# Kernel optimization log

Hardware: AMD Instinct MI355X
Metric: run time of the kernel (lower is better)

## Reference

```python
import jax, jax.numpy as jnp
import numpy as np

L = 128          # bandlimit (max_l)
NTHETA = 256     # Gauss-Legendre latitudes (>= L for exact quadrature)
NPHI = 512       # longitudes (>= 2L-1)
C_IN, C_OUT = 32, 32


def _normalized_assoc_legendre(Lmax, xg):
    """Pbar_lm(x) with Condon-Shortley phase, orthonormal on the sphere.
    Returns (Lmax, Lmax, T) for m>=0; zero for m>l."""
    T = xg.shape[0]
    P = np.zeros((Lmax, Lmax, T), dtype=np.float64)
    sx = np.sqrt(np.maximum(1.0 - xg * xg, 0.0))
    P[0, 0] = 1.0 / np.sqrt(4.0 * np.pi)
    for m in range(1, Lmax):
        P[m, m] = -np.sqrt((2 * m + 1) / (2.0 * m)) * sx * P[m - 1, m - 1]
    for m in range(0, Lmax - 1):
        P[m + 1, m] = np.sqrt(2 * m + 3.0) * xg * P[m, m]
    for m in range(Lmax):
        for l in range(m + 2, Lmax):
            a = np.sqrt((4.0 * l * l - 1.0) / (l * l - m * m))
            b = np.sqrt(((l - 1.0) ** 2 - m * m) / (4.0 * (l - 1.0) ** 2 - 1.0))
            P[l, m] = a * (xg * P[l - 1, m] - b * P[l - 2, m])
    return P


def _build_basis():
    # Gauss-Legendre quadrature in cos(theta): exact for degree <= 2*NTHETA-1
    xg, wg = np.polynomial.legendre.leggauss(NTHETA)
    P = _normalized_assoc_legendre(L, xg)  # (L, L, T), m>=0
    # Full basis B[l, m+L-1, t]; Pbar_{l,-m} = (-1)^m Pbar_{l,m}
    B = np.zeros((L, 2 * L - 1, NTHETA), dtype=np.float64)
    for m in range(-(L - 1), L):
        B[:, m + L - 1, :] = ((-1.0) ** abs(m) if m < 0 else 1.0) * P[:, abs(m), :]
    return B.astype(np.float32), wg.astype(np.float32)


def setup_inputs() -> dict:
    key = jax.random.key(0)
    k1, k2, k3 = jax.random.split(key, 3)
    x = jax.random.normal(k1, (NTHETA, NPHI, C_IN), dtype=jnp.float32)
    std = 1.0 / (C_IN + C_OUT)
    wr = std * jax.random.normal(k2, (L, 2 * L - 1, C_IN, C_OUT), dtype=jnp.float32)
    wi = std * jax.random.normal(k3, (L, 2 * L - 1, C_IN, C_OUT), dtype=jnp.float32)
    B, wg = _build_basis()
    return {"x": x, "weights_real": wr, "weights_imag": wi,
            "legendre": jnp.asarray(B), "quad_w": jnp.asarray(wg)}


def reference(x, weights_real, weights_imag, legendre, quad_w):
    ntheta, nphi, _ = x.shape
    Lb = legendre.shape[0]
    # --- forward SHT (per channel, vectorized) ---
    # longitude FFT: Fm[t,k,c] = sum_p x e^{-i 2pi k p / nphi}; dphi = 2pi/nphi
    Fm = jnp.fft.fft(x.astype(jnp.complex64), axis=1) * (2.0 * np.pi / nphi)
    midx = np.arange(-(Lb - 1), Lb) % nphi            # FFT bins for m=-(L-1)..L-1
    Fm_sel = Fm[:, midx, :]                           # (t, 2L-1, c)
    Bw = legendre * quad_w[None, None, :]             # quadrature-weighted basis
    # flm[l,m,c] = sum_t w_t Pbar_lm(theta_t) Fm[t,m,c]
    flm = jnp.einsum('lmt,tmc->lmc', Bw.astype(jnp.complex64), Fm_sel)
    # --- spectral conv: per-(l,m) channel mixing ---
    W = weights_real.astype(jnp.complex64) + 1j * weights_imag.astype(jnp.complex64)
    y = jnp.einsum('lmc,lmco->lmo', flm, W)           # (L, 2L-1, O)
    # --- inverse SHT ---
    G = jnp.einsum('lmt,lmo->tmo', legendre.astype(jnp.complex64), y)  # (t, 2L-1, O)
    spec = jnp.zeros((ntheta, nphi, G.shape[-1]), dtype=jnp.complex64)
    spec = spec.at[:, midx, :].set(G)
    out = jnp.fft.ifft(spec, axis=1) * nphi           # f = sum_m G e^{i m phi}
    return jnp.moveaxis(out.real, 2, 0)               # (O, ntheta, nphi)
```

## Files before the change

### kernel.cpp

```cpp
#include <hip/hip_runtime.h>
#include <math.h>

#define DEVFN __global__ __launch_bounds__(256)

namespace {
constexpr int LL  = 128;
constexpr int MM2 = 255;
constexpr int NT  = 256;
constexpr int NP  = 512;
constexpr int NC  = 32;
constexpr int NO  = 32;
constexpr float TWO_PI = 6.283185307179586476925286766559f;
}

typedef short v8s __attribute__((ext_vector_type(8)));
typedef float v4f __attribute__((ext_vector_type(4)));

__device__ inline unsigned short f2bf(float f) {
  unsigned int u = __float_as_uint(f);
  return (unsigned short)((u + 0x7FFFu + ((u >> 16) & 1u)) >> 16);
}

__device__ inline int m_of(int k, int mloc) {
  return (mloc < 8) ? (8 * k + mloc) : (120 - 8 * k + (mloc - 8));
}

DEVFN void kp_prep(const float* __restrict__ x, unsigned short* __restrict__ tw1t,
                   unsigned short* __restrict__ vt, unsigned short* __restrict__ xb) {
  __shared__ float sm[32][65];
  const int bid = blockIdx.x;
  const int tid = threadIdx.x;
  const float phi = TWO_PI / (float)NP;
  if (bid < 512) {
    const int idx = bid * 256 + tid;
    const float fs = TWO_PI / (float)NP;
    {
      const int n = idx >> 9, p = idx & 511;
      const int m = n >> 1;
      const int k = (m * p) & (NP - 1);
      float s, c;
      sincosf(phi * (float)k, &s, &c);
      tw1t[idx] = f2bf((n & 1) ? (-s * fs) : (c * fs));
    }
    {
      const int p = idx >> 8, k = idx & 255;
      const int m = k >> 1;
      const int kk = (m * p) & (NP - 1);
      float s, c;
      sincosf(phi * (float)kk, &s, &c);
      vt[idx] = f2bf((k & 1) ? s : c);
    }
  } else {
    const int q = bid - 512;
    const int t = q >> 3;
    const int p0 = (q & 7) * 64;
#pragma unroll
    for (int i = 0; i < 8; ++i) {
      const int idx = tid + i * 256;
      const int p = idx >> 5, c = idx & 31;
      sm[c][p] = x[((size_t)t * NP + p0 + p) * NC + c];
    }
    __syncthreads();
    const int c = tid >> 3, pg = tid & 7;
    unsigned short pk[8];
#pragma unroll
    for (int u = 0; u < 8; ++u) pk[u] = f2bf(sm[c][pg * 8 + u]);
    *(uint4*)(xb + ((size_t)(t * 32 + c)) * NP + p0 + pg * 8) = *(const uint4*)pk;
  }
}

DEVFN void k1_mfma(const unsigned short* __restrict__ xb,
                   const unsigned short* __restrict__ tw1t,
                   const float* __restrict__ wg,
                   float* __restrict__ fwr, float* __restrict__ fwi) {
  __shared__ unsigned short As[128 * 32];
  __shared__ unsigned short Bs[64 * 32];
  const int tid = threadIdx.x;
  const int r0 = blockIdx.x * 128;
  const int n0 = blockIdx.y * 64;
  const int wid = tid >> 6, lane = tid & 63;
  const int wm = wid & 1, wn = wid >> 1;
  v4f acc[4][2];
#pragma unroll
  for (int i = 0; i < 4; ++i)
#pragma unroll
    for (int j = 0; j < 2; ++j) {
      acc[i][j][0] = 0.f; acc[i][j][1] = 0.f; acc[i][j][2] = 0.f; acc[i][j][3] = 0.f;
    }
  const int lr = lane & 15, lk = (lane >> 4) * 8;
  for (int k0 = 0; k0 < 512; k0 += 32) {
#pragma unroll
    for (int s = 0; s < 3; ++s) {
      const int chunk = tid + s * 256;
      if (chunk < 512) {
        const int row = chunk >> 2, c16 = chunk & 3;
        *(uint4*)&As[row * 32 + c16 * 8] =
            *(const uint4*)&xb[(size_t)(r0 + row) * 512 + k0 + c16 * 8];
      } else {
        const int bc = chunk - 512;
        const int row = bc >> 2, c16 = bc & 3;
        *(uint4*)&Bs[row * 32 + c16 * 8] =
            *(const uint4*)&tw1t[(size_t)(n0 + row) * 512 + k0 + c16 * 8];
      }
    }
    __syncthreads();
    v8s af[4], bf[2];
#pragma unroll
    for (int i = 0; i < 4; ++i) af[i] = *(const v8s*)&As[(wm * 64 + i * 16 + lr) * 32 + lk];
#pragma unroll
    for (int j = 0; j < 2; ++j) bf[j] = *(const v8s*)&Bs[(wn * 32 + j * 16 + lr) * 32 + lk];
#pragma unroll
    for (int i = 0; i < 4; ++i)
#pragma unroll
      for (int j = 0; j < 2; ++j)
        acc[i][j] = __builtin_amdgcn_mfma_f32_16x16x32_bf16(af[i], bf[j], acc[i][j], 0, 0, 0);
    __syncthreads();
  }
  const int lrow = (lane >> 4) * 4;
#pragma unroll
  for (int i = 0; i < 4; ++i) {
    const int rbase = r0 + wm * 64 + i * 16 + lrow;
    const int t = rbase >> 5, c0 = rbase & 31;
    const float w = wg[t];
#pragma unroll
    for (int j = 0; j < 2; ++j) {
      const int n = n0 + wn * 32 + j * 16 + lr;
      const int mI = n >> 1;
      float* dst = (n & 1) ? fwi : fwr;
      float4 v = {acc[i][j][0] * w, acc[i][j][1] * w, acc[i][j][2] * w, acc[i][j][3] * w};
      *(float4*)&dst[((size_t)mI * NT + t) * NC + c0] = v;
    }
  }
}

DEVFN void k2_flm(const float* __restrict__ leg, const float* __restrict__ fwr,
                  const float* __restrict__ fwi, float* __restrict__ flr,
                  float* __restrict__ fli) {
  const int m  = blockIdx.x;
  const int l0 = m + blockIdx.y * 8 + (threadIdx.x >> 6) * 2;
  if (l0 >= LL) return;
  const int lane = threadIdx.x & 63;
  const int c = lane & 31;
  const int l1 = min(l0 + 1, LL - 1);
  const float* fp = ((lane >> 5) ? fwi : fwr) + (size_t)m * NT * NC + c;
  const float* lgA = leg + ((size_t)(l0 * MM2 + 127 + m)) * NT;
  const float* lgB = leg + ((size_t)(l1 * MM2 + 127 + m)) * NT;
  float a0 = 0.f, a1 = 0.f;
#pragma unroll 4
  for (int t = 0; t < NT; t += 4) {
    const float f0 = fp[(t + 0) * NC];
    const float f1 = fp[(t + 1) * NC];
    const float f2 = fp[(t + 2) * NC];
    const float f3 = fp[(t + 3) * NC];
    const float4 bA = *(const float4*)(lgA + t);
    const float4 bB = *(const float4*)(lgB + t);
    a0 = fmaf(bA.x, f0, a0); a0 = fmaf(bA.y, f1, a0);
    a0 = fmaf(bA.z, f2, a0); a0 = fmaf(bA.w, f3, a0);
    a1 = fmaf(bB.x, f0, a1); a1 = fmaf(bB.y, f1, a1);
    a1 = fmaf(bB.z, f2, a1); a1 = fmaf(bB.w, f3, a1);
  }
  float* outp = (lane >> 5) ? fli : flr;
  outp[(size_t)(m * LL + l0) * NC + c] = a0;
  if (l0 + 1 < LL) outp[(size_t)(m * LL + l0 + 1) * NC + c] = a1;
}

DEVFN void k3_mix(const float* __restrict__ flr, const float* __restrict__ fli,
                  const float* __restrict__ wr, const float* __restrict__ wi,
                  float* __restrict__ ya, float* __restrict__ yb) {
  const int m  = blockIdx.x;
  const int wid = threadIdx.x >> 6, lane = threadIdx.x & 63;
  const int l = m + blockIdx.y * 4 + wid;
  if (l >= LL) return;
  const int c8 = lane >> 3;
  const int o8 = lane & 7;
  const int c0 = c8 * 4, o0 = o8 * 4;
  const float s0 = (m > 0) ? 1.0f : 0.0f;
  const size_t rp = ((size_t)(l * MM2 + 127 + m) * NC) * NO;
  const size_t rn = ((size_t)(l * MM2 + 127 - m) * NC) * NO;
  const float4 fa4 = *(const float4*)&flr[(size_t)(m * LL + l) * NC + c0];
  const float4 fb4 = *(const float4*)&fli[(size_t)(m * LL + l) * NC + c0];
  float4 accA = {0.f, 0.f, 0.f, 0.f}, accB = {0.f, 0.f, 0.f, 0.f};
#pragma unroll
  for (int i = 0; i < 4; ++i) {
    const int c = c0 + i;
    const float4 wrp = *(const float4*)&wr[rp + (size_t)c * NO + o0];
    const float4 wrn = *(const float4*)&wr[rn + (size_t)c * NO + o0];
    const float4 wip = *(const float4*)&wi[rp + (size_t)c * NO + o0];
    const float4 win = *(const float4*)&wi[rn + (size_t)c * NO + o0];
    const float fa = (i == 0) ? fa4.x : (i == 1) ? fa4.y : (i == 2) ? fa4.z : fa4.w;
    const float fb = (i == 0) ? fb4.x : (i == 1) ? fb4.y : (i == 2) ? fb4.z : fb4.w;
    float4 wa, wb;
    wa.x = fmaf(s0, wrn.x, wrp.x); wa.y = fmaf(s0, wrn.y, wrp.y);
    wa.z = fmaf(s0, wrn.z, wrp.z); wa.w = fmaf(s0, wrn.w, wrp.w);
    wb.x = fmaf(s0, win.x, -wip.x); wb.y = fmaf(s0, win.y, -wip.y);
    wb.z = fmaf(s0, win.z, -wip.z); wb.w = fmaf(s0, win.w, -wip.w);
    accA.x = fmaf(fa, wa.x, fmaf(fb, wb.x, accA.x));
    accA.y = fmaf(fa, wa.y, fmaf(fb, wb.y, accA.y));
    accA.z = fmaf(fa, wa.z, fmaf(fb, wb.z, accA.z));
    accA.w = fmaf(fa, wa.w, fmaf(fb, wb.w, accA.w));
    accB.x = fmaf(fa, wb.x, fmaf(-fb, wa.x, accB.x));
    accB.y = fmaf(fa, wb.y, fmaf(-fb, wa.y, accB.y));
    accB.z = fmaf(fa, wb.z, fmaf(-fb, wa.z, accB.z));
    accB.w = fmaf(fa, wb.w, fmaf(-fb, wa.w, accB.w));
  }
#pragma unroll
  for (int mask = 8; mask <= 32; mask <<= 1) {
    accA.x += __shfl_xor(accA.x, mask); accA.y += __shfl_xor(accA.y, mask);
    accA.z += __shfl_xor(accA.z, mask); accA.w += __shfl_xor(accA.w, mask);
    accB.x += __shfl_xor(accB.x, mask); accB.y += __shfl_xor(accB.y, mask);
    accB.z += __shfl_xor(accB.z, mask); accB.w += __shfl_xor(accB.w, mask);
  }
  if (c8 == 0) {
    *(float4*)&ya[(size_t)(m * LL + l) * NO + o0] = accA;
    *(float4*)&yb[(size_t)(m * LL + l) * NO + o0] = accB;
  }
}

DEVFN void k4_G(const float* __restrict__ leg, const float* __restrict__ ya,
                const float* __restrict__ yb, unsigned short* __restrict__ ut) {
  const int fid = blockIdx.x + (int)blockIdx.y * 128;
  const int xk  = fid & 7;
  const int loc = fid >> 3;
  const int m   = m_of(xk, loc >> 3);
  const int tc  = loc & 7;
  const int o = threadIdx.x & 31;
  const int tq = threadIdx.x >> 5;
  const int t0 = tc * 32 + tq * 4;
  float aa[4] = {}, bb[4] = {};
#pragma unroll 4
  for (int l = m; l < LL; ++l) {
    const float4 g = *(const float4*)(leg + ((size_t)(l * MM2 + 127 + m)) * NT + t0);
    const float yav = ya[(m * LL + l) * NO + o];
    const float ybv = yb[(m * LL + l) * NO + o];
    aa[0] = fmaf(g.x, yav, aa[0]);  bb[0] = fmaf(g.x, ybv, bb[0]);
    aa[1] = fmaf(g.y, yav, aa[1]);  bb[1] = fmaf(g.y, ybv, bb[1]);
    aa[2] = fmaf(g.z, yav, aa[2]);  bb[2] = fmaf(g.z, ybv, bb[2]);
    aa[3] = fmaf(g.w, yav, aa[3]);  bb[3] = fmaf(g.w, ybv, bb[3]);
  }
#pragma unroll
  for (int i = 0; i < 4; ++i) {
    const unsigned int pk = (unsigned int)f2bf(aa[i]) | ((unsigned int)f2bf(bb[i]) << 16);
    *(unsigned int*)&ut[((size_t)((t0 + i) * 32 + o)) * 256 + 2 * m] = pk;
  }
}

DEVFN void k5_mfma(const unsigned short* __restrict__ ut,
                   const unsigned short* __restrict__ vt,
                   float* __restrict__ out) {
  __shared__ unsigned short As[128 * 32];
  __shared__ unsigned short Bs[128 * 32];
  const int tid = threadIdx.x;
  const int p0 = blockIdx.x * 128;
  const int r0 = blockIdx.y * 128;
  const int wid = tid >> 6, lane = tid & 63;
  const int wm = wid & 1, wn = wid >> 1;
  v4f acc[4][4];
#pragma unroll
  for (int i = 0; i < 4; ++i)
#pragma unroll
    for (int j = 0; j < 4; ++j) {
      acc[i][j][0] = 0.f; acc[i][j][1] = 0.f; acc[i][j][2] = 0.f; acc[i][j][3] = 0.f;
    }
  const int lr = lane & 15, lk = (lane >> 4) * 8;
  for (int k0 = 0; k0 < 256; k0 += 32) {
#pragma unroll
    for (int s = 0; s < 2; ++s) {
      const int chunk = tid + s * 256;
      const int row = chunk >> 2, c16 = chunk & 3;
      *(uint4*)&As[row * 32 + c16 * 8] =
          *(const uint4*)&vt[(size_t)(p0 + row) * 256 + k0 + c16 * 8];
      *(uint4*)&Bs[row * 32 + c16 * 8] =
          *(const uint4*)&ut[(size_t)(r0 + row) * 256 + k0 + c16 * 8];
    }
    __syncthreads();
    v8s af[4], bf[4];
#pragma unroll
    for (int i = 0; i < 4; ++i) af[i] = *(const v8s*)&As[(wm * 64 + i * 16 + lr) * 32 + lk];
#pragma unroll
    for (int j = 0; j < 4; ++j) bf[j] = *(const v8s*)&Bs[(wn * 64 + j * 16 + lr) * 32 + lk];
#pragma unroll
    for (int i = 0; i < 4; ++i)
#pragma unroll
      for (int j = 0; j < 4; ++j)
        acc[i][j] = __builtin_amdgcn_mfma_f32_16x16x32_bf16(af[i], bf[j], acc[i][j], 0, 0, 0);
    __syncthreads();
  }
  const int lrow = (lane >> 4) * 4;
#pragma unroll
  for (int i = 0; i < 4; ++i) {
    const int pbase = p0 + wm * 64 + i * 16 + lrow;
#pragma unroll
    for (int j = 0; j < 4; ++j) {
      const int r = r0 + wn * 64 + j * 16 + lr;
      const int t = r >> 5, o = r & 31;
      float4 v = {acc[i][j][0], acc[i][j][1], acc[i][j][2], acc[i][j][3]};
      *(float4*)&out[((size_t)o * NT + t) * NP + pbase] = v;
    }
  }
}

extern "C" void kernel_launch(void* const* d_in, const int* in_sizes, int n_in,
                              void* d_out, int out_size, void* d_ws, size_t ws_size,
                              hipStream_t stream) {
  const float* x   = (const float*)d_in[0];
  const float* wr  = (const float*)d_in[1];
  const float* wi  = (const float*)d_in[2];
  const float* leg = (const float*)d_in[3];
  const float* wg  = (const float*)d_in[4];
  float* out = (float*)d_out;

  unsigned short* tw1t = (unsigned short*)d_ws;
  unsigned short* vt   = tw1t + 131072;
  unsigned short* xb   = vt + 131072;
  unsigned short* ut   = xb + 4194304;
  float* fwr = (float*)(ut + 2097152);
  float* fwi = fwr + 1048576;
  float* flr = fwi + 1048576;
  float* fli = flr + 524288;
  float* ya  = fli + 524288;
  float* yb  = ya + 524288;

  hipLaunchKernelGGL(kp_prep, dim3(2560), dim3(256), 0, stream, x, tw1t, vt, xb);
  hipLaunchKernelGGL(k1_mfma, dim3(64, 4), dim3(256), 0, stream, xb, tw1t, wg, fwr, fwi);
  hipLaunchKernelGGL(k2_flm, dim3(128, 16), dim3(256), 0, stream, leg, fwr, fwi, flr, fli);
  hipLaunchKernelGGL(k3_mix, dim3(128, 32), dim3(256), 0, stream, flr, fli, wr, wi, ya, yb);
  hipLaunchKernelGGL(k4_G, dim3(128, 8), dim3(256), 0, stream, leg, ya, yb, ut);
  hipLaunchKernelGGL(k5_mfma, dim3(4, 64), dim3(256), 0, stream, ut, vt, out);
}
```

Baseline: 364.8 us.

## Fuse forward Legendre, channel mix and inverse Legendre into one kernel

Replaces the separate flm, mixing and G kernels with one kernel per (m, l-residue-mod-4) block that holds flm and y in shared memory. The inverse Legendre partial sums for the four l-residue groups go to four fp32 slabs. The final MFMA kernel reduces these slabs and converts them to bf16 while staging its B tile. That kernel also changes its tile shape to 256x64. This removes two launches and the global round-trips for flm and y, at the cost of 4x partial-sum traffic. Each block's inner loop also runs longer and more serially, and with one block per (m, residue) and no triangle reordering, work per block is uneven across m.

New measurement: 417.7 us. 1.15x slower.

```diff
diff --git a/kernel.cpp b/kernel.cpp
--- a/kernel.cpp
+++ b/kernel.cpp
@@ -19,10 +19,6 @@
 __device__ inline unsigned short f2bf(float f) {
   unsigned int u = __float_as_uint(f);
   return (unsigned short)((u + 0x7FFFu + ((u >> 16) & 1u)) >> 16);
-}
-
-__device__ inline int m_of(int k, int mloc) {
-  return (mloc < 8) ? (8 * k + mloc) : (120 - 8 * k + (mloc - 8));
 }
 
 DEVFN void kp_prep(const float* __restrict__ x, unsigned short* __restrict__ tw1t,
@@ -133,127 +129,131 @@
   }
 }
 
-DEVFN void k2_flm(const float* __restrict__ leg, const float* __restrict__ fwr,
-                  const float* __restrict__ fwi, float* __restrict__ flr,
-                  float* __restrict__ fli) {
-  const int m  = blockIdx.x;
-  const int l0 = m + blockIdx.y * 8 + (threadIdx.x >> 6) * 2;
-  if (l0 >= LL) return;
-  const int lane = threadIdx.x & 63;
-  const int c = lane & 31;
-  const int l1 = min(l0 + 1, LL - 1);
-  const float* fp = ((lane >> 5) ? fwi : fwr) + (size_t)m * NT * NC + c;
-  const float* lgA = leg + ((size_t)(l0 * MM2 + 127 + m)) * NT;
-  const float* lgB = leg + ((size_t)(l1 * MM2 + 127 + m)) * NT;
-  float a0 = 0.f, a1 = 0.f;
-#pragma unroll 4
-  for (int t = 0; t < NT; t += 4) {
-    const float f0 = fp[(t + 0) * NC];
-    const float f1 = fp[(t + 1) * NC];
-    const float f2 = fp[(t + 2) * NC];
-    const float f3 = fp[(t + 3) * NC];
-    const float4 bA = *(const float4*)(lgA + t);
-    const float4 bB = *(const float4*)(lgB + t);
-    a0 = fmaf(bA.x, f0, a0); a0 = fmaf(bA.y, f1, a0);
-    a0 = fmaf(bA.z, f2, a0); a0 = fmaf(bA.w, f3, a0);
-    a1 = fmaf(bB.x, f0, a1); a1 = fmaf(bB.y, f1, a1);
-    a1 = fmaf(bB.z, f2, a1); a1 = fmaf(bB.w, f3, a1);
-  }
-  float* outp = (lane >> 5) ? fli : flr;
-  outp[(size_t)(m * LL + l0) * NC + c] = a0;
-  if (l0 + 1 < LL) outp[(size_t)(m * LL + l0 + 1) * NC + c] = a1;
-}
-
-DEVFN void k3_mix(const float* __restrict__ flr, const float* __restrict__ fli,
-                  const float* __restrict__ wr, const float* __restrict__ wi,
-                  float* __restrict__ ya, float* __restrict__ yb) {
-  const int m  = blockIdx.x;
-  const int wid = threadIdx.x >> 6, lane = threadIdx.x & 63;
-  const int l = m + blockIdx.y * 4 + wid;
-  if (l >= LL) return;
-  const int c8 = lane >> 3;
-  const int o8 = lane & 7;
-  const int c0 = c8 * 4, o0 = o8 * 4;
-  const float s0 = (m > 0) ? 1.0f : 0.0f;
-  const size_t rp = ((size_t)(l * MM2 + 127 + m) * NC) * NO;
-  const size_t rn = ((size_t)(l * MM2 + 127 - m) * NC) * NO;
-  const float4 fa4 = *(const float4*)&flr[(size_t)(m * LL + l) * NC + c0];
-  const float4 fb4 = *(const float4*)&fli[(size_t)(m * LL + l) * NC + c0];
-  float4 accA = {0.f, 0.f, 0.f, 0.f}, accB = {0.f, 0.f, 0.f, 0.f};
-#pragma unroll
-  for (int i = 0; i < 4; ++i) {
-    const int c = c0 + i;
-    const float4 wrp = *(const float4*)&wr[rp + (size_t)c * NO + o0];
-    const float4 wrn = *(const float4*)&wr[rn + (size_t)c * NO + o0];
-    const float4 wip = *(const float4*)&wi[rp + (size_t)c * NO + o0];
-    const float4 win = *(const float4*)&wi[rn + (size_t)c * NO + o0];
-    const float fa = (i == 0) ? fa4.x : (i == 1) ? fa4.y : (i == 2) ? fa4.z : fa4.w;
-    const float fb = (i == 0) ? fb4.x : (i == 1) ? fb4.y : (i == 2) ? fb4.z : fb4.w;
-    float4 wa, wb;
-    wa.x = fmaf(s0, wrn.x, wrp.x); wa.y = fmaf(s0, wrn.y, wrp.y);
-    wa.z = fmaf(s0, wrn.z, wrp.z); wa.w = fmaf(s0, wrn.w, wrp.w);
-    wb.x = fmaf(s0, win.x, -wip.x); wb.y = fmaf(s0, win.y, -wip.y);
-    wb.z = fmaf(s0, win.z, -wip.z); wb.w = fmaf(s0, win.w, -wip.w);
-    accA.x = fmaf(fa, wa.x, fmaf(fb, wb.x, accA.x));
-    accA.y = fmaf(fa, wa.y, fmaf(fb, wb.y, accA.y));
-    accA.z = fmaf(fa, wa.z, fmaf(fb, wb.z, accA.z));
-    accA.w = fmaf(fa, wa.w, fmaf(fb, wb.w, accA.w));
-    accB.x = fmaf(fa, wb.x, fmaf(-fb, wa.x, accB.x));
-    accB.y = fmaf(fa, wb.y, fmaf(-fb, wa.y, accB.y));
-    accB.z = fmaf(fa, wb.z, fmaf(-fb, wa.z, accB.z));
-    accB.w = fmaf(fa, wb.w, fmaf(-fb, wa.w, accB.w));
-  }
-#pragma unroll
-  for (int mask = 8; mask <= 32; mask <<= 1) {
-    accA.x += __shfl_xor(accA.x, mask); accA.y += __shfl_xor(accA.y, mask);
-    accA.z += __shfl_xor(accA.z, mask); accA.w += __shfl_xor(accA.w, mask);
-    accB.x += __shfl_xor(accB.x, mask); accB.y += __shfl_xor(accB.y, mask);
-    accB.z += __shfl_xor(accB.z, mask); accB.w += __shfl_xor(accB.w, mask);
-  }
-  if (c8 == 0) {
-    *(float4*)&ya[(size_t)(m * LL + l) * NO + o0] = accA;
-    *(float4*)&yb[(size_t)(m * LL + l) * NO + o0] = accB;
-  }
-}
-
-DEVFN void k4_G(const float* __restrict__ leg, const float* __restrict__ ya,
-                const float* __restrict__ yb, unsigned short* __restrict__ ut) {
-  const int fid = blockIdx.x + (int)blockIdx.y * 128;
-  const int xk  = fid & 7;
-  const int loc = fid >> 3;
-  const int m   = m_of(xk, loc >> 3);
-  const int tc  = loc & 7;
-  const int o = threadIdx.x & 31;
-  const int tq = threadIdx.x >> 5;
-  const int t0 = tc * 32 + tq * 4;
-  float aa[4] = {}, bb[4] = {};
-#pragma unroll 4
-  for (int l = m; l < LL; ++l) {
-    const float4 g = *(const float4*)(leg + ((size_t)(l * MM2 + 127 + m)) * NT + t0);
-    const float yav = ya[(m * LL + l) * NO + o];
-    const float ybv = yb[(m * LL + l) * NO + o];
-    aa[0] = fmaf(g.x, yav, aa[0]);  bb[0] = fmaf(g.x, ybv, bb[0]);
-    aa[1] = fmaf(g.y, yav, aa[1]);  bb[1] = fmaf(g.y, ybv, bb[1]);
-    aa[2] = fmaf(g.z, yav, aa[2]);  bb[2] = fmaf(g.z, ybv, bb[2]);
-    aa[3] = fmaf(g.w, yav, aa[3]);  bb[3] = fmaf(g.w, ybv, bb[3]);
-  }
-#pragma unroll
-  for (int i = 0; i < 4; ++i) {
-    const unsigned int pk = (unsigned int)f2bf(aa[i]) | ((unsigned int)f2bf(bb[i]) << 16);
-    *(unsigned int*)&ut[((size_t)((t0 + i) * 32 + o)) * 256 + 2 * m] = pk;
-  }
-}
-
-DEVFN void k5_mfma(const unsigned short* __restrict__ ut,
+__global__ __launch_bounds__(256, 2) void k23B(
+    const float* __restrict__ leg, const float* __restrict__ fwr,
+    const float* __restrict__ fwi, const float* __restrict__ wr,
+    const float* __restrict__ wi, float* __restrict__ gp) {
+  __shared__ float sflm[32][64];
+  __shared__ float sy[32][64];
+  const int bid = blockIdx.x;
+  const int m = bid >> 2, q = bid & 3;
+  const int tid = threadIdx.x;
+  const int wid = tid >> 6, lane = tid & 63;
+  const int jmin = (m > q) ? ((m - q + 3) >> 2) : 0;
+
+  {
+    const int c = lane & 31;
+    const float* fp = ((lane >> 5) ? fwi : fwr) + (size_t)m * NT * NC + c;
+    const float* lg[8];
+#pragma unroll
+    for (int k = 0; k < 8; ++k) {
+      const int l = q + 4 * (wid + 4 * k);
+      lg[k] = leg + ((size_t)(l * MM2 + 127 + m)) * NT;
+    }
+    float acc[8] = {};
+    for (int t = 0; t < NT; t += 4) {
+      const float f0 = fp[(t + 0) * NC];
+      const float f1 = fp[(t + 1) * NC];
+      const float f2 = fp[(t + 2) * NC];
+      const float f3 = fp[(t + 3) * NC];
+#pragma unroll
+      for (int k = 0; k < 8; ++k) {
+        const float4 b = *(const float4*)(lg[k] + t);
+        acc[k] = fmaf(b.x, f0, acc[k]);
+        acc[k] = fmaf(b.y, f1, acc[k]);
+        acc[k] = fmaf(b.z, f2, acc[k]);
+        acc[k] = fmaf(b.w, f3, acc[k]);
+      }
+    }
+#pragma unroll
+    for (int k = 0; k < 8; ++k) sflm[wid + 4 * k][lane] = acc[k];
+  }
+  __syncthreads();
+
+  {
+    const int c8 = lane >> 3, o8 = lane & 7;
+    const int c0 = c8 * 4, o0 = o8 * 4;
+    const float s0 = (m > 0) ? 1.0f : 0.0f;
+    for (int k = 0; k < 8; ++k) {
+      const int j = wid + 4 * k;
+      const int l = q + 4 * j;
+      if (l < m) continue;
+      const size_t rp = ((size_t)(l * MM2 + 127 + m) * NC) * NO;
+      const size_t rn = ((size_t)(l * MM2 + 127 - m) * NC) * NO;
+      float4 accA = {0.f, 0.f, 0.f, 0.f}, accB = {0.f, 0.f, 0.f, 0.f};
+#pragma unroll
+      for (int i = 0; i < 4; ++i) {
+        const int c = c0 + i;
+        const float4 wrp = *(const float4*)&wr[rp + (size_t)c * NO + o0];
+        const float4 wrn = *(const float4*)&wr[rn + (size_t)c * NO + o0];
+        const float4 wip = *(const float4*)&wi[rp + (size_t)c * NO + o0];
+        const float4 win = *(const float4*)&wi[rn + (size_t)c * NO + o0];
+        const float fa = sflm[j][c];
+        const float fb = sflm[j][32 + c];
+        float4 wa, wb;
+        wa.x = fmaf(s0, wrn.x, wrp.x); wa.y = fmaf(s0, wrn.y, wrp.y);
+        wa.z = fmaf(s0, wrn.z, wrp.z); wa.w = fmaf(s0, wrn.w, wrp.w);
+        wb.x = fmaf(s0, win.x, -wip.x); wb.y = fmaf(s0, win.y, -wip.y);
+        wb.z = fmaf(s0, win.z, -wip.z); wb.w = fmaf(s0, win.w, -wip.w);
+        accA.x = fmaf(fa, wa.x, fmaf(fb, wb.x, accA.x));
+        accA.y = fmaf(fa, wa.y, fmaf(fb, wb.y, accA.y));
+        accA.z = fmaf(fa, wa.z, fmaf(fb, wb.z, accA.z));
+        accA.w = fmaf(fa, wa.w, fmaf(fb, wb.w, accA.w));
+        accB.x = fmaf(fa, wb.x, fmaf(-fb, wa.x, accB.x));
+        accB.y = fmaf(fa, wb.y, fmaf(-fb, wa.y, accB.y));
+        accB.z = fmaf(fa, wb.z, fmaf(-fb, wa.z, accB.z));
+        accB.w = fmaf(fa, wb.w, fmaf(-fb, wa.w, accB.w));
+      }
+#pragma unroll
+      for (int mask = 8; mask <= 32; mask <<= 1) {
+        accA.x += __shfl_xor(accA.x, mask); accA.y += __shfl_xor(accA.y, mask);
+        accA.z += __shfl_xor(accA.z, mask); accA.w += __shfl_xor(accA.w, mask);
+        accB.x += __shfl_xor(accB.x, mask); accB.y += __shfl_xor(accB.y, mask);
+        accB.z += __shfl_xor(accB.z, mask); accB.w += __shfl_xor(accB.w, mask);
+      }
+      if (c8 == 0) {
+        *(float4*)&sy[j][o0] = accA;
+        *(float4*)&sy[j][32 + o0] = accB;
+      }
+    }
+  }
+  __syncthreads();
+
+  {
+    const int o = tid & 31, tq = tid >> 5;
+    float* gq = gp + (size_t)q * (256 * 8192);
+    for (int w = 0; w < 8; ++w) {
+      const int t0 = w * 32 + tq * 4;
+      float aa[4] = {}, bb[4] = {};
+      for (int j = jmin; j < 32; ++j) {
+        const int l = q + 4 * j;
+        const float4 g = *(const float4*)(leg + ((size_t)(l * MM2 + 127 + m)) * NT + t0);
+        const float yav = sy[j][o];
+        const float ybv = sy[j][32 + o];
+        aa[0] = fmaf(g.x, yav, aa[0]);  bb[0] = fmaf(g.x, ybv, bb[0]);
+        aa[1] = fmaf(g.y, yav, aa[1]);  bb[1] = fmaf(g.y, ybv, bb[1]);
+        aa[2] = fmaf(g.z, yav, aa[2]);  bb[2] = fmaf(g.z, ybv, bb[2]);
+        aa[3] = fmaf(g.w, yav, aa[3]);  bb[3] = fmaf(g.w, ybv, bb[3]);
+      }
+#pragma unroll
+      for (int i = 0; i < 4; ++i) {
+        const size_t rr = (size_t)(t0 + i) * 32 + o;
+        gq[(size_t)(2 * m) * 8192 + rr] = aa[i];
+        gq[(size_t)(2 * m + 1) * 8192 + rr] = bb[i];
+      }
+    }
+  }
+}
+
+DEVFN void k5_mfma(const float* __restrict__ gp,
                    const unsigned short* __restrict__ vt,
                    float* __restrict__ out) {
-  __shared__ unsigned short As[128 * 32];
-  __shared__ unsigned short Bs[128 * 32];
+  __shared__ unsigned short As[256 * 32];
+  __shared__ unsigned short Bs[64 * 32];
   const int tid = threadIdx.x;
-  const int p0 = blockIdx.x * 128;
-  const int r0 = blockIdx.y * 128;
+  const int p0 = blockIdx.x * 256;
+  const int r0 = blockIdx.y * 64;
   const int wid = tid >> 6, lane = tid & 63;
-  const int wm = wid & 1, wn = wid >> 1;
   v4f acc[4][4];
 #pragma unroll
   for (int i = 0; i < 4; ++i)
@@ -262,22 +262,38 @@
       acc[i][j][0] = 0.f; acc[i][j][1] = 0.f; acc[i][j][2] = 0.f; acc[i][j][3] = 0.f;
     }
   const int lr = lane & 15, lk = (lane >> 4) * 8;
+  const int ke = tid >> 3, rq = tid & 7;
   for (int k0 = 0; k0 < 256; k0 += 32) {
 #pragma unroll
-    for (int s = 0; s < 2; ++s) {
-      const int chunk = tid + s * 256;
-      const int row = chunk >> 2, c16 = chunk & 3;
+    for (int s = 0; s < 4; ++s) {
+      const int unit = tid + s * 256;
+      const int row = unit >> 2, c16 = unit & 3;
       *(uint4*)&As[row * 32 + c16 * 8] =
           *(const uint4*)&vt[(size_t)(p0 + row) * 256 + k0 + c16 * 8];
-      *(uint4*)&Bs[row * 32 + c16 * 8] =
-          *(const uint4*)&ut[(size_t)(r0 + row) * 256 + k0 + c16 * 8];
+    }
+    {
+      const size_t base = (size_t)(k0 + ke) * 8192 + r0 + rq * 8;
+      float4 s0 = *(const float4*)&gp[base];
+      float4 s1 = *(const float4*)&gp[base + 4];
+#pragma unroll
+      for (int qq = 1; qq < 4; ++qq) {
+        const size_t qb = (size_t)qq * (256 * 8192) + base;
+        const float4 a0 = *(const float4*)&gp[qb];
+        const float4 a1 = *(const float4*)&gp[qb + 4];
+        s0.x += a0.x; s0.y += a0.y; s0.z += a0.z; s0.w += a0.w;
+        s1.x += a1.x; s1.y += a1.y; s1.z += a1.z; s1.w += a1.w;
+      }
+      const unsigned short h[8] = {f2bf(s0.x), f2bf(s0.y), f2bf(s0.z), f2bf(s0.w),
+                                   f2bf(s1.x), f2bf(s1.y), f2bf(s1.z), f2bf(s1.w)};
+#pragma unroll
+      for (int i = 0; i < 8; ++i) Bs[(rq * 8 + i) * 32 + ke] = h[i];
     }
     __syncthreads();
     v8s af[4], bf[4];
 #pragma unroll
-    for (int i = 0; i < 4; ++i) af[i] = *(const v8s*)&As[(wm * 64 + i * 16 + lr) * 32 + lk];
-#pragma unroll
-    for (int j = 0; j < 4; ++j) bf[j] = *(const v8s*)&Bs[(wn * 64 + j * 16 + lr) * 32 + lk];
+    for (int i = 0; i < 4; ++i) af[i] = *(const v8s*)&As[(wid * 64 + i * 16 + lr) * 32 + lk];
+#pragma unroll
+    for (int j = 0; j < 4; ++j) bf[j] = *(const v8s*)&Bs[(j * 16 + lr) * 32 + lk];
 #pragma unroll
     for (int i = 0; i < 4; ++i)
 #pragma unroll
@@ -288,10 +304,10 @@
   const int lrow = (lane >> 4) * 4;
 #pragma unroll
   for (int i = 0; i < 4; ++i) {
-    const int pbase = p0 + wm * 64 + i * 16 + lrow;
+    const int pbase = p0 + wid * 64 + i * 16 + lrow;
 #pragma unroll
     for (int j = 0; j < 4; ++j) {
-      const int r = r0 + wn * 64 + j * 16 + lr;
+      const int r = r0 + j * 16 + lr;
       const int t = r >> 5, o = r & 31;
       float4 v = {acc[i][j][0], acc[i][j][1], acc[i][j][2], acc[i][j][3]};
       *(float4*)&out[((size_t)o * NT + t) * NP + pbase] = v;
@@ -312,18 +328,12 @@
   unsigned short* tw1t = (unsigned short*)d_ws;
   unsigned short* vt   = tw1t + 131072;
   unsigned short* xb   = vt + 131072;
-  unsigned short* ut   = xb + 4194304;
-  float* fwr = (float*)(ut + 2097152);
+  float* fwr = (float*)(xb + 4194304);
   float* fwi = fwr + 1048576;
-  float* flr = fwi + 1048576;
-  float* fli = flr + 524288;
-  float* ya  = fli + 524288;
-  float* yb  = ya + 524288;
+  float* gp  = fwi + 1048576;
 
   hipLaunchKernelGGL(kp_prep, dim3(2560), dim3(256), 0, stream, x, tw1t, vt, xb);
   hipLaunchKernelGGL(k1_mfma, dim3(64, 4), dim3(256), 0, stream, xb, tw1t, wg, fwr, fwi);
-  hipLaunchKernelGGL(k2_flm, dim3(128, 16), dim3(256), 0, stream, leg, fwr, fwi, flr, fli);
-  hipLaunchKernelGGL(k3_mix, dim3(128, 32), dim3(256), 0, stream, flr, fli, wr, wi, ya, yb);
-  hipLaunchKernelGGL(k4_G, dim3(128, 8), dim3(256), 0, stream, leg, ya, yb, ut);
-  hipLaunchKernelGGL(k5_mfma, dim3(4, 64), dim3(256), 0, stream, ut, vt, out);
-}
+  hipLaunchKernelGGL(k23B, dim3(512), dim3(256), 0, stream, leg, fwr, fwi, wr, wi, gp);
+  hipLaunchKernelGGL(k5_mfma, dim3(2, 128), dim3(256), 0, stream, gp, vt, out);
+}
```
